# Optimization experiments

Hardware: AMD Instinct MI355X
Metric: run time of the kernel (lower is better)

The kernel has to match this reference:

```python
import jax, jax.numpy as jnp
import numpy as np

LN_EPS = 1e-5

def _layer_norm(x, g, b):
    mu = jnp.mean(x, axis=-1, keepdims=True)
    var = jnp.mean(jnp.square(x - mu), axis=-1, keepdims=True)
    return (x - mu) * jax.lax.rsqrt(var + LN_EPS) * g + b

def _conv(x, src, tgt, N, alphas, ws, W3, W_self, bias, deg_power):
    # alphas, ws: tuples of 3 per-edge [E] arrays (sp, ctx, lat)
    # W3: [3, in, out]; deg_power: [3]
    out = x @ W_self + bias  # self loop + bias, [N, out]
    for c in range(3):
        eff = alphas[c] * ws[c]                                   # [E]
        deg = jnp.ones((N,), x.dtype).at[tgt].add(eff)            # [N]
        dinv = jnp.power(jnp.clip(deg, 1e-6), deg_power[c])       # [N]
        norm = eff * dinv[tgt] * dinv[src]                        # [E]
        h = x @ W3[c]                                             # [N, out] (linear => transform before gather)
        msg = norm[:, None] * h[src]                              # [E, out]
        out = out + jax.ops.segment_sum(msg, tgt, num_segments=N)
    return out

def setup_inputs() -> dict:
    N, E, D, L = 50000, 1000000, 128, 2
    key = jax.random.key(0)
    ks = jax.random.split(key, 16)
    scale = 1.0 / np.sqrt(D)
    inp = {
        "x": jax.random.normal(ks[0], (N, D), jnp.float32),
        "edge_index": jax.random.randint(ks[1], (2, E), 0, N, jnp.int32),
        "alpha_sp": jax.random.uniform(ks[2], (E,), jnp.float32),
        "alpha_ctx": jax.random.uniform(ks[3], (E,), jnp.float32),
        "alpha_lat": jax.random.uniform(ks[4], (E,), jnp.float32),
        "w_sp": jax.random.uniform(ks[5], (E,), jnp.float32),
        "w_ctx": jax.random.uniform(ks[6], (E,), jnp.float32),
        "w_lat": jax.random.uniform(ks[7], (E,), jnp.float32),
        # stacked per-layer params: [L, 3, in, out] for the three channel weights
        "W3": jax.random.normal(ks[8], (L, 3, D, D), jnp.float32) * scale,
        "W_self": jax.random.normal(ks[9], (L, D, D), jnp.float32) * scale,
        "bias": jnp.zeros((L, D), jnp.float32),
        "deg_power": jnp.full((L, 3), -0.5, jnp.float32),
        "ln_g": jnp.ones((D,), jnp.float32),
        "ln_b": jnp.zeros((D,), jnp.float32),
        "num_nodes": N,
    }
    return inp

def reference(x, edge_index, alpha_sp, alpha_ctx, alpha_lat, w_sp, w_ctx, w_lat,
              W3, W_self, bias, deg_power, ln_g, ln_b, num_nodes):
    N = num_nodes
    src, tgt = edge_index[0], edge_index[1]
    alphas = (alpha_sp, alpha_ctx, alpha_lat)
    ws = (w_sp, w_ctx, w_lat)
    L = W3.shape[0]
    h = x
    for i in range(L):
        h = _conv(h, src, tgt, N, alphas, ws, W3[i], W_self[i], bias[i], deg_power[i])
        if i < L - 1:
            h = _layer_norm(h, ln_g, ln_b)
            h = jax.nn.relu(h)
            # dropout: eval mode (identity)
    return h
```

## Files before the change

### kernel.cpp

```cpp
#include <hip/hip_runtime.h>
#include <hip/hip_bf16.h>

typedef short bf16x8 __attribute__((ext_vector_type(8)));
typedef float f32x4 __attribute__((ext_vector_type(4)));

#define BSH 7
#define BK  (1 << BSH)

static inline int cdiv(int a, int b){ return (a + b - 1) / b; }

__device__ __forceinline__ unsigned pack_bf16_hi(float v){
    return ((unsigned)__bfloat16_as_ushort(__float2bfloat16(v))) << 16;
}
__device__ __forceinline__ float bf16hi_to_f32(unsigned bits_hi16){
    return __uint_as_float(bits_hi16);
}

__global__ __launch_bounds__(256) void k_bcnt0(const int* __restrict__ tgt,
                                               int* __restrict__ gcnt, int E, int NB){
    __shared__ int lh[1024];
    int tid = threadIdx.x;
    for (int b = tid; b < 1024; b += 256) lh[b] = 0;
    __syncthreads();
    int c0 = blockIdx.x * 4096;
    #pragma unroll
    for (int u = 0; u < 16; ++u){
        int e = c0 + u * 256 + tid;
        if (e < E) atomicAdd(&lh[tgt[e] >> BSH], 1);
    }
    __syncthreads();
    for (int b = tid; b < NB; b += 256){
        int c = lh[b];
        if (c) atomicAdd(&gcnt[b], c);
    }
}

__global__ __launch_bounds__(256) void k_bscan(const int* __restrict__ gcnt,
                                               int* __restrict__ bbase,
                                               int* __restrict__ gcur,
                                               int* __restrict__ rs,
                                               int N, int E){
    __shared__ int sc[256];
    int tid = threadIdx.x;
    int b0 = tid * 4;
    int v0 = gcnt[b0], v1 = gcnt[b0 + 1], v2 = gcnt[b0 + 2], v3 = gcnt[b0 + 3];
    int t3 = v0 + v1 + v2 + v3;
    sc[tid] = t3;
    __syncthreads();
    for (int off = 1; off < 256; off <<= 1){
        int x = (tid >= off) ? sc[tid - off] : 0;
        __syncthreads();
        sc[tid] += x;
        __syncthreads();
    }
    int ex = sc[tid] - t3;
    bbase[b0]     = ex;
    bbase[b0 + 1] = ex + v0;
    bbase[b0 + 2] = ex + v0 + v1;
    bbase[b0 + 3] = ex + v0 + v1 + v2;
    gcur[b0] = bbase[b0]; gcur[b0 + 1] = bbase[b0 + 1];
    gcur[b0 + 2] = bbase[b0 + 2]; gcur[b0 + 3] = bbase[b0 + 3];
    if (tid == 255) bbase[1024] = sc[255];
    if (tid == 0)   rs[N] = E;
}

__global__ __launch_bounds__(256) void k_bin(
        const int* __restrict__ src, const int* __restrict__ tgt,
        const float* __restrict__ asp, const float* __restrict__ actx,
        const float* __restrict__ alat, const float* __restrict__ wsp,
        const float* __restrict__ wctx, const float* __restrict__ wlat,
        int* __restrict__ gcur, uint4* __restrict__ binned, int E, int NB){
    __shared__ int lh[1024], lo[1024], lc[1024], gb[1024], tsum[256];
    __shared__ unsigned sx[4096], sy[4096];
    __shared__ int st[4096];
    int tid = threadIdx.x;
    int c0 = blockIdx.x * 4096;
    int cnt = E - c0; if (cnt > 4096) cnt = 4096;
    for (int b = tid; b < 1024; b += 256){ lh[b] = 0; lc[b] = 0; }
    __syncthreads();
    #pragma unroll
    for (int u = 0; u < 16; ++u){
        int e = c0 + u * 256 + tid;
        if (e < E) atomicAdd(&lh[tgt[e] >> BSH], 1);
    }
    __syncthreads();
    int b4 = tid * 4;
    int v0 = lh[b4], v1 = lh[b4 + 1], v2 = lh[b4 + 2], v3 = lh[b4 + 3];
    int t3 = v0 + v1 + v2 + v3;
    tsum[tid] = t3;
    __syncthreads();
    for (int off = 1; off < 256; off <<= 1){
        int x = (tid >= off) ? tsum[tid - off] : 0;
        __syncthreads();
        tsum[tid] += x;
        __syncthreads();
    }
    int ex = tsum[tid] - t3;
    lo[b4] = ex; lo[b4 + 1] = ex + v0; lo[b4 + 2] = ex + v0 + v1; lo[b4 + 3] = ex + v0 + v1 + v2;
    for (int b = tid; b < NB; b += 256){
        int c = lh[b];
        gb[b] = c ? atomicAdd(&gcur[b], c) : 0;
    }
    __syncthreads();
    #pragma unroll
    for (int u = 0; u < 16; ++u){
        int e = c0 + u * 256 + tid;
        if (e < E){
            int t = tgt[e];
            int b = t >> BSH;
            int p = lo[b] + atomicAdd(&lc[b], 1);
            sx[p] = (unsigned)src[e] | pack_bf16_hi(asp[e] * wsp[e]);
            sy[p] = (pack_bf16_hi(actx[e] * wctx[e]) >> 16) | pack_bf16_hi(alat[e] * wlat[e]);
            st[p] = t;
        }
    }
    __syncthreads();
    for (int i = tid; i < cnt; i += 256){
        int t = st[i];
        int b = t >> BSH;
        int g = gb[b] + (i - lo[b]);
        uint4 o = {sx[i], sy[i], (unsigned)t, 0u};
        binned[g] = o;
    }
}

__global__ __launch_bounds__(256) void k_bucket(
        const uint4* __restrict__ binned, const int* __restrict__ bbase,
        uint2* __restrict__ effo, int* __restrict__ rs, int N){
    __shared__ int th[128], sc2[128], cur[128];
    int tid = threadIdx.x;
    int b = blockIdx.x;
    int t0 = b << BSH;
    int ebeg = bbase[b], eend = bbase[b + 1];
    if (tid < 128) th[tid] = 0;
    __syncthreads();
    for (int i = ebeg + tid; i < eend; i += 256)
        atomicAdd(&th[(int)binned[i].z - t0], 1);
    __syncthreads();
    int v = (tid < 128) ? th[tid] : 0;
    if (tid < 128) sc2[tid] = v;
    __syncthreads();
    for (int off = 1; off < 128; off <<= 1){
        int x = (tid >= off && tid < 128) ? sc2[tid - off] : 0;
        __syncthreads();
        if (tid < 128) sc2[tid] += x;
        __syncthreads();
    }
    if (tid < 128){
        int exv = sc2[tid] - v;
        cur[tid] = exv;
        int t = t0 + tid;
        if (t < N) rs[t] = ebeg + exv;
    }
    __syncthreads();
    for (int i = ebeg + tid; i < eend; i += 256){
        uint4 r = binned[i];
        int loc = (int)r.z - t0;
        int p = atomicAdd(&cur[loc], 1);
        uint2 o = {r.x, r.y};
        effo[ebeg + p] = o;
    }
}

__global__ __launch_bounds__(256) void k_deg(
        const uint2* __restrict__ effo, const int* __restrict__ rs,
        const float* __restrict__ dp,
        float* __restrict__ dinv_all,
        int N, int L){
    int n = blockIdx.x * 256 + threadIdx.x;
    if (n >= N) return;
    int beg = rs[n], end = rs[n + 1];
    float s0 = 0.f, s1 = 0.f, s2 = 0.f;
    for (int i = beg; i < end; ++i){
        uint2 v = effo[i];
        s0 += bf16hi_to_f32(v.x & 0xFFFF0000u);
        s1 += bf16hi_to_f32(v.y << 16);
        s2 += bf16hi_to_f32(v.y & 0xFFFF0000u);
    }
    float d0 = fmaxf(1.f + s0, 1e-6f);
    float d1 = fmaxf(1.f + s1, 1e-6f);
    float d2 = fmaxf(1.f + s2, 1e-6f);
    for (int l = 0; l < L; ++l){
        size_t base = ((size_t)l * N + n) * 3;
        dinv_all[base + 0] = powf(d0, dp[l * 3 + 0]);
        dinv_all[base + 1] = powf(d1, dp[l * 3 + 1]);
        dinv_all[base + 2] = powf(d2, dp[l * 3 + 2]);
    }
}

__global__ void k_normv(const uint2* __restrict__ effo,
                        const float* __restrict__ dinv_all,
                        uint2* __restrict__ nv, int E, int N, int L){
    int i = blockIdx.x * 256 + threadIdx.x;
    if (i >= L * E) return;
    int l = i / E;
    int e = i - l * E;
    const float* dinv = dinv_all + (size_t)l * N * 3;
    uint2 v = effo[e];
    unsigned s = v.x & 0xFFFFu;
    float e0 = bf16hi_to_f32(v.x & 0xFFFF0000u);
    float e1 = bf16hi_to_f32(v.y << 16);
    float e2 = bf16hi_to_f32(v.y & 0xFFFF0000u);
    float n0 = e0 * dinv[3 * s + 0];
    float n1 = e1 * dinv[3 * s + 1];
    float n2 = e2 * dinv[3 * s + 2];
    uint2 o;
    o.x = s | pack_bf16_hi(n0);
    o.y = (pack_bf16_hi(n1) >> 16) | pack_bf16_hi(n2);
    nv[i] = o;
}

__global__ void k_x2bf(const float* __restrict__ x, __hip_bfloat16* __restrict__ Ap, int n){
    int i = blockIdx.x * 256 + threadIdx.x;
    if (i < n) Ap[(size_t)(i >> 7) * 512 + (i & 127)] = __float2bfloat16(x[i]);
}

__global__ void k_wcat(const float* __restrict__ Wself,
                       const float* __restrict__ W3,
                       __hip_bfloat16* __restrict__ BT,
                       int L){
    int i = blockIdx.x * 256 + threadIdx.x;
    if (i >= L * 65536) return;
    int l = i >> 16, r = i & 65535;
    int j = r >> 9, k = r & 511;
    float v;
    if (k < 128) v = Wself[l * 16384 + k * 128 + j];
    else {
        int c = (k >> 7) - 1, kk = k & 127;
        v = W3[l * 49152 + (c * 128 + kk) * 128 + j];
    }
    BT[i] = __float2bfloat16(v);
}

__global__ __launch_bounds__(256) void k_msg(
        __hip_bfloat16* __restrict__ Ap,
        const uint2* __restrict__ nv,
        const int* __restrict__ rs,
        const float* __restrict__ dinv,
        int N){
    int w = threadIdx.x >> 6, lane = threadIdx.x & 63;
    int t = blockIdx.x * 4 + w;
    if (t >= N) return;
    float ax0 = 0.f, ay0 = 0.f, ax1 = 0.f, ay1 = 0.f, ax2 = 0.f, ay2 = 0.f;
    int beg = rs[t], end = rs[t + 1];
    int i = beg;
    for (; i + 8 <= end; i += 8){
        uint2 m[8];
        #pragma unroll
        for (int u = 0; u < 8; ++u) m[u] = nv[i + u];
        float2 f[8];
        #pragma unroll
        for (int u = 0; u < 8; ++u){
            const __hip_bfloat162* p =
                (const __hip_bfloat162*)(Ap + (size_t)(m[u].x & 0xFFFFu) * 512);
            f[u] = __bfloat1622float2(p[lane]);
        }
        #pragma unroll
        for (int u = 0; u < 8; ++u){
            float n0 = bf16hi_to_f32(m[u].x & 0xFFFF0000u);
            float n1 = bf16hi_to_f32(m[u].y << 16);
            float n2 = bf16hi_to_f32(m[u].y & 0xFFFF0000u);
            ax0 += n0 * f[u].x; ay0 += n0 * f[u].y;
            ax1 += n1 * f[u].x; ay1 += n1 * f[u].y;
            ax2 += n2 * f[u].x; ay2 += n2 * f[u].y;
        }
    }
    for (; i < end; ++i){
        uint2 m = nv[i];
        const __hip_bfloat162* p =
            (const __hip_bfloat162*)(Ap + (size_t)(m.x & 0xFFFFu) * 512);
        float2 fv = __bfloat1622float2(p[lane]);
        float n0 = bf16hi_to_f32(m.x & 0xFFFF0000u);
        float n1 = bf16hi_to_f32(m.y << 16);
        float n2 = bf16hi_to_f32(m.y & 0xFFFF0000u);
        ax0 += n0 * fv.x; ay0 += n0 * fv.y;
        ax1 += n1 * fv.x; ay1 += n1 * fv.y;
        ax2 += n2 * fv.x; ay2 += n2 * fv.y;
    }
    float dt0 = dinv[3 * t], dt1 = dinv[3 * t + 1], dt2 = dinv[3 * t + 2];
    __hip_bfloat162* yo = (__hip_bfloat162*)(Ap + (size_t)t * 512 + 128) + lane;
    float2 r0 = {dt0 * ax0, dt0 * ay0};
    float2 r1 = {dt1 * ax1, dt1 * ay1};
    float2 r2 = {dt2 * ax2, dt2 * ay2};
    yo[0]   = __float22bfloat162_rn(r0);
    yo[64]  = __float22bfloat162_rn(r1);
    yo[128] = __float22bfloat162_rn(r2);
}

__global__ __launch_bounds__(256) void k_gemm(
        const __hip_bfloat16* __restrict__ A,
        const __hip_bfloat16* __restrict__ BT,
        const float* __restrict__ bias,
        float* __restrict__ outbuf,
        int M){
    __shared__ __hip_bfloat16 As[128 * 128];
    __shared__ __hip_bfloat16 Bs[128 * 128];
    const int tid = threadIdx.x;
    const int row0 = blockIdx.x * 128;
    const int w = tid >> 6, lane = tid & 63;
    const int wm = (w & 1) * 64, wn = (w >> 1) * 64;
    const int lm = lane & 15, lq = lane >> 4;

    f32x4 acc[4][4];
    #pragma unroll
    for (int mt = 0; mt < 4; ++mt)
        #pragma unroll
        for (int nt = 0; nt < 4; ++nt)
            acc[mt][nt] = {0.f, 0.f, 0.f, 0.f};

    for (int kt = 0; kt < 4; ++kt){
        #pragma unroll
        for (int it = 0; it < 8; ++it){
            int v = it * 256 + tid;
            int r = v >> 4, c = v & 15;
            int soff = r * 128 + ((c ^ (r & 15)) << 3);
            int4 av = {0, 0, 0, 0};
            if (row0 + r < M)
                av = *(const int4*)(A + (size_t)(row0 + r) * 512 + kt * 128 + (c << 3));
            *(int4*)(&As[soff]) = av;
            int4 bv = *(const int4*)(BT + (size_t)r * 512 + kt * 128 + (c << 3));
            *(int4*)(&Bs[soff]) = bv;
        }
        __syncthreads();

        #pragma unroll
        for (int kk = 0; kk < 4; ++kk){
            int kc = kk * 4 + lq;
            bf16x8 a[4], b[4];
            #pragma unroll
            for (int mt = 0; mt < 4; ++mt){
                int r = wm + mt * 16 + lm;
                a[mt] = *(const bf16x8*)(&As[r * 128 + ((kc ^ (r & 15)) << 3)]);
            }
            #pragma unroll
            for (int nt = 0; nt < 4; ++nt){
                int r = wn + nt * 16 + lm;
                b[nt] = *(const bf16x8*)(&Bs[r * 128 + ((kc ^ (r & 15)) << 3)]);
            }
            #pragma unroll
            for (int mt = 0; mt < 4; ++mt)
                #pragma unroll
                for (int nt = 0; nt < 4; ++nt)
                    acc[mt][nt] = __builtin_amdgcn_mfma_f32_16x16x32_bf16(
                        a[mt], b[nt], acc[mt][nt], 0, 0, 0);
        }
        __syncthreads();
    }

    #pragma unroll
    for (int mt = 0; mt < 4; ++mt){
        #pragma unroll
        for (int nt = 0; nt < 4; ++nt){
            int col = wn + nt * 16 + lm;
            #pragma unroll
            for (int r = 0; r < 4; ++r){
                int row = row0 + wm + mt * 16 + lq * 4 + r;
                if (row < M)
                    outbuf[(size_t)row * 128 + col] = acc[mt][nt][r] + bias[col];
            }
        }
    }
}

__global__ __launch_bounds__(256) void k_ln(
        const float* __restrict__ outbuf,
        const float* __restrict__ g,
        const float* __restrict__ b,
        __hip_bfloat16* __restrict__ Ap, int N){
    int w = threadIdx.x >> 6, lane = threadIdx.x & 63;
    int t = blockIdx.x * 4 + w;
    if (t >= N) return;
    const float* row = outbuf + (size_t)t * 128;
    float x0 = row[2 * lane], x1 = row[2 * lane + 1];
    float s = x0 + x1;
    #pragma unroll
    for (int off = 32; off; off >>= 1) s += __shfl_xor(s, off);
    float mu = s * (1.0f / 128.0f);
    float d0 = x0 - mu, d1 = x1 - mu;
    float ss = d0 * d0 + d1 * d1;
    #pragma unroll
    for (int off = 32; off; off >>= 1) ss += __shfl_xor(ss, off);
    float r = rsqrtf(ss * (1.0f / 128.0f) + 1e-5f);
    float y0 = fmaxf(d0 * r * g[2 * lane]     + b[2 * lane],     0.0f);
    float y1 = fmaxf(d1 * r * g[2 * lane + 1] + b[2 * lane + 1], 0.0f);
    float2 y = {y0, y1};
    *((__hip_bfloat162*)(Ap + (size_t)t * 512) + lane) = __float22bfloat162_rn(y);
}

extern "C" void kernel_launch(void* const* d_in, const int* in_sizes, int n_in,
                              void* d_out, int out_size, void* d_ws, size_t ws_size,
                              hipStream_t stream) {
    const float* x     = (const float*)d_in[0];
    const int*   ei    = (const int*)d_in[1];
    const float* asp   = (const float*)d_in[2];
    const float* actx  = (const float*)d_in[3];
    const float* alat  = (const float*)d_in[4];
    const float* wsp   = (const float*)d_in[5];
    const float* wctx  = (const float*)d_in[6];
    const float* wlat  = (const float*)d_in[7];
    const float* W3    = (const float*)d_in[8];
    const float* Wself = (const float*)d_in[9];
    const float* bias  = (const float*)d_in[10];
    const float* dpow  = (const float*)d_in[11];
    const float* lng   = (const float*)d_in[12];
    const float* lnb   = (const float*)d_in[13];

    const int N = in_sizes[0] / 128;
    const int E = in_sizes[1] / 2;
    const int L = in_sizes[8] / (3 * 128 * 128);
    const int NB = cdiv(N, BK);
    const int* src = ei;
    const int* tgt = ei + E;

    char* p = (char*)d_ws;
    auto alloc = [&](size_t bytes) -> void* {
        void* r = (void*)p;
        p += (bytes + 255) & ~(size_t)255;
        return r;
    };
    int*   rs       = (int*)  alloc((size_t)(N + 1) * 4);
    int*   gcnt     = (int*)  alloc(1024 * 4);
    int*   bbase    = (int*)  alloc(1025 * 4);
    int*   gcur     = (int*)  alloc(1024 * 4);
    uint2* effo     = (uint2*)alloc((size_t)E * 8);
    uint2* nv       = (uint2*)alloc((size_t)L * E * 8);
    float* dinv_all = (float*)alloc((size_t)L * N * 3 * 4);
    float* outbuf   = (float*)alloc((size_t)N * 128 * 4);
    __hip_bfloat16* Ap = (__hip_bfloat16*)alloc((size_t)N * 512 * 2);
    __hip_bfloat16* BT = (__hip_bfloat16*)alloc((size_t)L * 128 * 512 * 2);
    uint4* binned = (uint4*)nv;

    hipMemsetAsync(gcnt, 0, 1024 * 4, stream);
    k_bcnt0 <<<cdiv(E, 4096), 256, 0, stream>>>(tgt, gcnt, E, NB);
    k_bscan <<<1, 256, 0, stream>>>(gcnt, bbase, gcur, rs, N, E);
    k_bin   <<<cdiv(E, 4096), 256, 0, stream>>>(src, tgt, asp, actx, alat, wsp, wctx, wlat,
                                                gcur, binned, E, NB);
    k_bucket<<<NB, 256, 0, stream>>>(binned, bbase, effo, rs, N);
    k_deg   <<<cdiv(N, 256), 256, 0, stream>>>(effo, rs, dpow, dinv_all, N, L);
    k_x2bf  <<<cdiv(N * 128, 256), 256, 0, stream>>>(x, Ap, N * 128);
    k_wcat  <<<cdiv(L * 65536, 256), 256, 0, stream>>>(Wself, W3, BT, L);
    k_normv <<<cdiv(L * E, 256), 256, 0, stream>>>(effo, dinv_all, nv, E, N, L);

    for (int l = 0; l < L; ++l){
        float* obuf = (l == L - 1) ? (float*)d_out : outbuf;
        const float* dinv_l = dinv_all + (size_t)l * N * 3;
        k_msg <<<cdiv(N, 4), 256, 0, stream>>>(Ap, nv + (size_t)l * E, rs, dinv_l, N);
        k_gemm<<<cdiv(N, 128), 256, 0, stream>>>(Ap, BT + (size_t)l * 65536,
                                                 bias + l * 128, obuf, N);
        if (l < L - 1)
            k_ln<<<cdiv(N, 4), 256, 0, stream>>>(obuf, lng, lnb, Ap, N);
    }
}
```

Baseline: 371.1 us.

## Fuse LayerNorm+ReLU into GEMM epilogue and deepen message gather unroll

The GEMM epilogue now computes per-row mean and variance through shared-memory partial sums and writes the normalized, ReLU'd bf16 activations straight into the next layer's input buffer. This removes the separate LN kernel and the fp32 intermediate round trip. The message aggregation loop is unrolled to 16 edges with a 4-edge remainder loop to expose more outstanding gathers. Variance now uses E[x^2]-mu^2, which is slightly less numerically stable, and the GEMM writes Ap while other blocks may still be reading Ap as GEMM input.

```diff
diff --git a/kernel.cpp b/kernel.cpp
--- a/kernel.cpp
+++ b/kernel.cpp
@@ -244,19 +244,40 @@
     float ax0 = 0.f, ay0 = 0.f, ax1 = 0.f, ay1 = 0.f, ax2 = 0.f, ay2 = 0.f;
     int beg = rs[t], end = rs[t + 1];
     int i = beg;
-    for (; i + 8 <= end; i += 8){
-        uint2 m[8];
-        #pragma unroll
-        for (int u = 0; u < 8; ++u) m[u] = nv[i + u];
-        float2 f[8];
-        #pragma unroll
-        for (int u = 0; u < 8; ++u){
+    for (; i + 16 <= end; i += 16){
+        uint2 m[16];
+        #pragma unroll
+        for (int u = 0; u < 16; ++u) m[u] = nv[i + u];
+        float2 f[16];
+        #pragma unroll
+        for (int u = 0; u < 16; ++u){
             const __hip_bfloat162* p =
                 (const __hip_bfloat162*)(Ap + (size_t)(m[u].x & 0xFFFFu) * 512);
             f[u] = __bfloat1622float2(p[lane]);
         }
         #pragma unroll
-        for (int u = 0; u < 8; ++u){
+        for (int u = 0; u < 16; ++u){
+            float n0 = bf16hi_to_f32(m[u].x & 0xFFFF0000u);
+            float n1 = bf16hi_to_f32(m[u].y << 16);
+            float n2 = bf16hi_to_f32(m[u].y & 0xFFFF0000u);
+            ax0 += n0 * f[u].x; ay0 += n0 * f[u].y;
+            ax1 += n1 * f[u].x; ay1 += n1 * f[u].y;
+            ax2 += n2 * f[u].x; ay2 += n2 * f[u].y;
+        }
+    }
+    for (; i + 4 <= end; i += 4){
+        uint2 m[4];
+        #pragma unroll
+        for (int u = 0; u < 4; ++u) m[u] = nv[i + u];
+        float2 f[4];
+        #pragma unroll
+        for (int u = 0; u < 4; ++u){
+            const __hip_bfloat162* p =
+                (const __hip_bfloat162*)(Ap + (size_t)(m[u].x & 0xFFFFu) * 512);
+            f[u] = __bfloat1622float2(p[lane]);
+        }
+        #pragma unroll
+        for (int u = 0; u < 4; ++u){
             float n0 = bf16hi_to_f32(m[u].x & 0xFFFF0000u);
             float n1 = bf16hi_to_f32(m[u].y << 16);
             float n2 = bf16hi_to_f32(m[u].y & 0xFFFF0000u);
@@ -292,7 +313,9 @@
         const __hip_bfloat16* __restrict__ BT,
         const float* __restrict__ bias,
         float* __restrict__ outbuf,
-        int M){
+        int M, int doLN,
+        const float* __restrict__ g, const float* __restrict__ b,
+        __hip_bfloat16* __restrict__ Ap){
     __shared__ __hip_bfloat16 As[128 * 128];
     __shared__ __hip_bfloat16 Bs[128 * 128];
     const int tid = threadIdx.x;
@@ -326,7 +349,7 @@
         #pragma unroll
         for (int kk = 0; kk < 4; ++kk){
             int kc = kk * 4 + lq;
-            bf16x8 a[4], b[4];
+            bf16x8 a[4], b2[4];
             #pragma unroll
             for (int mt = 0; mt < 4; ++mt){
                 int r = wm + mt * 16 + lm;
@@ -335,56 +358,95 @@
             #pragma unroll
             for (int nt = 0; nt < 4; ++nt){
                 int r = wn + nt * 16 + lm;
-                b[nt] = *(const bf16x8*)(&Bs[r * 128 + ((kc ^ (r & 15)) << 3)]);
+                b2[nt] = *(const bf16x8*)(&Bs[r * 128 + ((kc ^ (r & 15)) << 3)]);
             }
             #pragma unroll
             for (int mt = 0; mt < 4; ++mt)
                 #pragma unroll
                 for (int nt = 0; nt < 4; ++nt)
                     acc[mt][nt] = __builtin_amdgcn_mfma_f32_16x16x32_bf16(
-                        a[mt], b[nt], acc[mt][nt], 0, 0, 0);
-        }
-        __syncthreads();
-    }
-
-    #pragma unroll
-    for (int mt = 0; mt < 4; ++mt){
+                        a[mt], b2[nt], acc[mt][nt], 0, 0, 0);
+        }
+        __syncthreads();
+    }
+
+    if (!doLN){
+        #pragma unroll
+        for (int mt = 0; mt < 4; ++mt){
+            #pragma unroll
+            for (int nt = 0; nt < 4; ++nt){
+                int col = wn + nt * 16 + lm;
+                #pragma unroll
+                for (int r = 0; r < 4; ++r){
+                    int row = row0 + wm + mt * 16 + lq * 4 + r;
+                    if (row < M)
+                        outbuf[(size_t)row * 128 + col] = acc[mt][nt][r] + bias[col];
+                }
+            }
+        }
+    } else {
+        float* S1 = (float*)As;
+        float* S2 = S1 + 4096;
+        float* MS = (float*)Bs;
+        const int half = wn >> 6;
+        const int slot = half * 16 + lm;
+        float bv[4];
+        #pragma unroll
+        for (int nt = 0; nt < 4; ++nt) bv[nt] = bias[wn + nt * 16 + lm];
+        #pragma unroll
+        for (int mt = 0; mt < 4; ++mt){
+            #pragma unroll
+            for (int r = 0; r < 4; ++r){
+                int rl = wm + mt * 16 + lq * 4 + r;
+                float ps = 0.f, pq = 0.f;
+                #pragma unroll
+                for (int nt = 0; nt < 4; ++nt){
+                    float v = acc[mt][nt][r] + bv[nt];
+                    ps += v; pq += v * v;
+                }
+                S1[rl * 32 + slot] = ps;
+                S2[rl * 32 + slot] = pq;
+            }
+        }
+        __syncthreads();
+        if (tid < 128){
+            float s = 0.f, sq = 0.f;
+            #pragma unroll
+            for (int j = 0; j < 32; ++j){
+                s  += S1[tid * 32 + j];
+                sq += S2[tid * 32 + j];
+            }
+            float mu = s * (1.0f / 128.0f);
+            float var = sq * (1.0f / 128.0f) - mu * mu;
+            MS[tid] = mu;
+            MS[128 + tid] = rsqrtf(var + 1e-5f);
+        }
+        __syncthreads();
+        float gv[4], bbv[4];
         #pragma unroll
         for (int nt = 0; nt < 4; ++nt){
             int col = wn + nt * 16 + lm;
+            gv[nt] = g[col]; bbv[nt] = b[col];
+        }
+        #pragma unroll
+        for (int mt = 0; mt < 4; ++mt){
             #pragma unroll
             for (int r = 0; r < 4; ++r){
-                int row = row0 + wm + mt * 16 + lq * 4 + r;
-                if (row < M)
-                    outbuf[(size_t)row * 128 + col] = acc[mt][nt][r] + bias[col];
+                int rl = wm + mt * 16 + lq * 4 + r;
+                int row = row0 + rl;
+                if (row < M){
+                    float mu = MS[rl], sc = MS[128 + rl];
+                    #pragma unroll
+                    for (int nt = 0; nt < 4; ++nt){
+                        int col = wn + nt * 16 + lm;
+                        float v = acc[mt][nt][r] + bv[nt];
+                        float y = fmaxf((v - mu) * sc * gv[nt] + bbv[nt], 0.0f);
+                        Ap[(size_t)row * 512 + col] = __float2bfloat16(y);
+                    }
+                }
             }
         }
     }
-}
-
-__global__ __launch_bounds__(256) void k_ln(
-        const float* __restrict__ outbuf,
-        const float* __restrict__ g,
-        const float* __restrict__ b,
-        __hip_bfloat16* __restrict__ Ap, int N){
-    int w = threadIdx.x >> 6, lane = threadIdx.x & 63;
-    int t = blockIdx.x * 4 + w;
-    if (t >= N) return;
-    const float* row = outbuf + (size_t)t * 128;
-    float x0 = row[2 * lane], x1 = row[2 * lane + 1];
-    float s = x0 + x1;
-    #pragma unroll
-    for (int off = 32; off; off >>= 1) s += __shfl_xor(s, off);
-    float mu = s * (1.0f / 128.0f);
-    float d0 = x0 - mu, d1 = x1 - mu;
-    float ss = d0 * d0 + d1 * d1;
-    #pragma unroll
-    for (int off = 32; off; off >>= 1) ss += __shfl_xor(ss, off);
-    float r = rsqrtf(ss * (1.0f / 128.0f) + 1e-5f);
-    float y0 = fmaxf(d0 * r * g[2 * lane]     + b[2 * lane],     0.0f);
-    float y1 = fmaxf(d1 * r * g[2 * lane + 1] + b[2 * lane + 1], 0.0f);
-    float2 y = {y0, y1};
-    *((__hip_bfloat162*)(Ap + (size_t)t * 512) + lane) = __float22bfloat162_rn(y);
 }
 
 extern "C" void kernel_launch(void* const* d_in, const int* in_sizes, int n_in,
@@ -425,7 +487,6 @@
     uint2* effo     = (uint2*)alloc((size_t)E * 8);
     uint2* nv       = (uint2*)alloc((size_t)L * E * 8);
     float* dinv_all = (float*)alloc((size_t)L * N * 3 * 4);
-    float* outbuf   = (float*)alloc((size_t)N * 128 * 4);
     __hip_bfloat16* Ap = (__hip_bfloat16*)alloc((size_t)N * 512 * 2);
     __hip_bfloat16* BT = (__hip_bfloat16*)alloc((size_t)L * 128 * 512 * 2);
     uint4* binned = (uint4*)nv;
@@ -442,12 +503,11 @@
     k_normv <<<cdiv(L * E, 256), 256, 0, stream>>>(effo, dinv_all, nv, E, N, L);
 
     for (int l = 0; l < L; ++l){
-        float* obuf = (l == L - 1) ? (float*)d_out : outbuf;
+        int doLN = (l < L - 1) ? 1 : 0;
         const float* dinv_l = dinv_all + (size_t)l * N * 3;
         k_msg <<<cdiv(N, 4), 256, 0, stream>>>(Ap, nv + (size_t)l * E, rs, dinv_l, N);
         k_gemm<<<cdiv(N, 128), 256, 0, stream>>>(Ap, BT + (size_t)l * 65536,
-                                                 bias + l * 128, obuf, N);
-        if (l < L - 1)
-            k_ln<<<cdiv(N, 4), 256, 0, stream>>>(obuf, lng, lnb, Ap, N);
-    }
-}
+                                                 bias + l * 128, (float*)d_out, N,
+                                                 doLN, lng, lnb, Ap);
+    }
+}
```

After: 363.8 us. 1.02x faster.
